# Kernel optimization log

Hardware: AMD Instinct MI355X
Metric: run time of the kernel (lower is better)

The kernel has to match this reference:

```python
import jax, jax.numpy as jnp
import numpy as np

B, S, D, H, DH, FF = 2, 2048, 1024, 16, 64, 4096
EPS = 1e-6


def setup_inputs() -> dict:
    key = jax.random.key(0)
    ks = jax.random.split(key, 12)
    s = lambda fan: 1.0 / np.sqrt(fan)
    return {
        "x": jax.random.normal(ks[0], (B, S, D), dtype=jnp.float32),
        "mask": jax.random.randint(ks[1], (B, S), 0, 2).astype(bool),
        "Wq": jax.random.normal(ks[2], (D, H * DH), dtype=jnp.float32) * s(D),
        "Wk": jax.random.normal(ks[3], (D, H * DH), dtype=jnp.float32) * s(D),
        "Wv": jax.random.normal(ks[4], (D, H * DH), dtype=jnp.float32) * s(D),
        "Wo": jax.random.normal(ks[5], (H * DH, D), dtype=jnp.float32) * s(H * DH),
        "bo": jnp.zeros((D,), dtype=jnp.float32),
        "W1": jax.random.normal(ks[6], (D, FF), dtype=jnp.float32) * s(D),
        "b1": jnp.zeros((FF,), dtype=jnp.float32),
        "W2": jax.random.normal(ks[7], (FF, D), dtype=jnp.float32) * s(FF),
        "b2": jnp.zeros((D,), dtype=jnp.float32),
        "g1": jnp.ones((D,), dtype=jnp.float32),   # layer_norm1 target_std
        "m1": jnp.zeros((D,), dtype=jnp.float32),  # layer_norm1 target_mean
        "g2": jnp.ones((D,), dtype=jnp.float32),
        "m2": jnp.zeros((D,), dtype=jnp.float32),
    }


def layer_norm(x, g, m):
    mu = jnp.mean(x, axis=-1, keepdims=True)
    xc = x - mu
    std = jnp.sqrt(jnp.mean(xc * xc, axis=-1, keepdims=True) + EPS)
    return g * xc / std + m


def reference(x, mask, Wq, Wk, Wv, Wo, bo, W1, b1, W2, b2, g1, m1, g2, m2):
    # --- multi-head self-attention (no proj bias) ---
    q = (x @ Wq).reshape(B, S, H, DH)
    k = (x @ Wk).reshape(B, S, H, DH)
    v = (x @ Wv).reshape(B, S, H, DH)
    scores = jnp.einsum("bqhd,bkhd->bhqk", q, k) / np.sqrt(DH)  # [B,H,S,S]
    scores = jnp.where(mask[:, None, None, :], -jnp.inf, scores)
    att = jax.nn.softmax(scores, axis=-1)
    ctx = jnp.einsum("bhqk,bkhd->bqhd", att, v).reshape(B, S, H * DH)
    attn_out = ctx @ Wo + bo
    # --- post-LN residual block (pre_ln=False, dropouts=0 in eval) ---
    x1 = layer_norm(attn_out + x, g1, m1)
    ff = jax.nn.relu(x1 @ W1 + b1) @ W2 + b2
    return layer_norm(ff + x1, g2, m2)
```

## Files before the change

### kernel.cpp

```cpp
#include <hip/hip_runtime.h>
#include <hip/hip_bf16.h>


typedef __bf16 bf16;
typedef __bf16 bf16x8 __attribute__((ext_vector_type(8)));
typedef __bf16 bf16x4 __attribute__((ext_vector_type(4)));
typedef float  f32x4  __attribute__((ext_vector_type(4)));
typedef float  f32x16 __attribute__((ext_vector_type(16)));
typedef unsigned u32x2 __attribute__((ext_vector_type(2)));
typedef unsigned u32x4 __attribute__((ext_vector_type(4)));

#define DEVI __device__ __forceinline__

constexpr int S_LEN  = 2048;
constexpr int NTOK   = 4096;
constexpr int DMODEL = 1024;
constexpr int NFF    = 4096;
constexpr float SCALE2 = 0.125f * 1.44269504088896f;
constexpr float MASKV2 = -30000.0f;

DEVI void gld16(const void* g, void* l) {
  __builtin_amdgcn_global_load_lds((const __attribute__((address_space(1))) void*)g,
                                   (__attribute__((address_space(3))) void*)l, 16, 0, 0);
}

DEVI f32x4 mfma16(bf16x8 a, bf16x8 b, f32x4 c) {
  return __builtin_amdgcn_mfma_f32_16x16x32_bf16(a, b, c, 0, 0, 0);
}
DEVI f32x16 mfma32(bf16x8 a, bf16x8 b, f32x16 c) {
  return __builtin_amdgcn_mfma_f32_32x32x16_bf16(a, b, c, 0, 0, 0);
}
DEVI unsigned cvtpk(float lo, float hi) {
  unsigned d;
  asm("v_cvt_pk_bf16_f32 %0, %1, %2" : "=v"(d) : "v"(lo), "v"(hi));
  return d;
}
DEVI void plswap(unsigned &a, unsigned &b) {
#if __has_builtin(__builtin_amdgcn_permlane32_swap)
  u32x2 r = __builtin_amdgcn_permlane32_swap(a, b, false, false);
  a = r[0]; b = r[1];
#else
  asm volatile("v_permlane32_swap_b32 %0, %1" : "+v"(a), "+v"(b));
#endif
}
DEVI float fexp2(float x) {
#if __has_builtin(__builtin_amdgcn_exp2f)
  return __builtin_amdgcn_exp2f(x);
#else
  return exp2f(x);
#endif
}
#define M3(a, b, c) fmaxf(fmaxf(a, b), c)

template <int MODE>
__global__ __launch_bounds__(256) void gemm_bt(
    const bf16* __restrict__ A, const bf16* __restrict__ Bt,
    void* __restrict__ out, const float* __restrict__ bias,
    int M, int N, int ld, int Kc, int nx, int ny)
{
  __shared__ bf16 As[128 * 32];
  __shared__ bf16 Bs[128 * 32];
  const int tid  = threadIdx.x;
  const int lane = tid & 63, w = tid >> 6;
  const int wr = w >> 1, wc = w & 1;

  const int id  = blockIdx.x;
  const int xcd = id & 7;
  int t2 = id >> 3;
  const int bx = t2 % nx;  t2 /= nx;
  const int ppx = ny >> 3;
  const int kz = t2 / ppx;
  const int by = xcd * ppx + (t2 % ppx);
  const int brow = by * 128, bcol = bx * 128;

  const bf16* Ag = A  + (size_t)(brow + w * 32 + (lane >> 2)) * ld + kz * Kc + (lane & 3) * 8;
  const bf16* Bg = Bt + (size_t)(bcol + w * 32 + (lane >> 2)) * ld + kz * Kc + (lane & 3) * 8;
  bf16* AsW = As + w * 1024;
  bf16* BsW = Bs + w * 1024;

  f32x4 acc[4][4] = {};

  for (int k0 = 0; k0 < Kc; k0 += 32) {
    gld16(Ag + k0,                    AsW);
    gld16(Ag + k0 + (size_t)16 * ld,  AsW + 512);
    gld16(Bg + k0,                    BsW);
    gld16(Bg + k0 + (size_t)16 * ld,  BsW + 512);
    __syncthreads();

    bf16x8 af[4], bfr[4];
#pragma unroll
    for (int m = 0; m < 4; ++m)
      af[m] = *(const bf16x8*)&As[(wr * 64 + m * 16 + (lane & 15)) * 32 + (lane >> 4) * 8];
#pragma unroll
    for (int n = 0; n < 4; ++n)
      bfr[n] = *(const bf16x8*)&Bs[(wc * 64 + n * 16 + (lane & 15)) * 32 + (lane >> 4) * 8];
    __builtin_amdgcn_s_setprio(1);
#pragma unroll
    for (int m = 0; m < 4; ++m)
#pragma unroll
      for (int n = 0; n < 4; ++n)
        acc[m][n] = mfma16(af[m], bfr[n], acc[m][n]);
    __builtin_amdgcn_s_setprio(0);
    __syncthreads();
  }

  const size_t plane = (size_t)NTOK * DMODEL;
#pragma unroll
  for (int m = 0; m < 4; ++m)
#pragma unroll
    for (int n = 0; n < 4; ++n)
#pragma unroll
      for (int r = 0; r < 4; ++r) {
        const int row = brow + wr * 64 + m * 16 + (lane >> 4) * 4 + r;
        const int col = bcol + wc * 64 + n * 16 + (lane & 15);
        const float v = acc[m][n][r];
        if (MODE == 0) {
          const int b = row >> 11, s = row & 2047;
          const int which = col >> 10, c = col & 1023, h = c >> 6, d = c & 63;
          bf16* qkv = (bf16*)out;
          if (which == 0)
            qkv[(((size_t)(b * 16 + h)) * 2048 + s) * 64 + d] = (bf16)(v * SCALE2);
          else if (which == 1)
            (qkv + plane)[(((size_t)(b * 16 + h)) * 2048 + s) * 64 + d] = (bf16)v;
          else
            (qkv + 2 * plane)[(((size_t)(b * 16 + h)) * 64 + d) * 2048 + s] = (bf16)v;
        } else if (MODE == 3) {
          const float t = v + bias[col];
          ((bf16*)out)[(size_t)row * N + col] = (bf16)fmaxf(t, 0.0f);
        } else {
          ((float*)out)[(size_t)kz * M * N + (size_t)row * N + col] = v;
        }
      }
}

__global__ __launch_bounds__(512) void attn_k(
    const bf16* __restrict__ q, const bf16* __restrict__ k,
    const bf16* __restrict__ vt, const unsigned* __restrict__ mbits,
    bf16* __restrict__ ctx)
{
  __shared__ __align__(16) char smem[36864];
  bf16* Kl = (bf16*)smem;
  bf16* Vl = (bf16*)(smem + 16384);
  const int tid = threadIdx.x, lane = tid & 63, w = tid >> 6;
  const int hi = lane >> 5, li = lane & 31;
  const int id = blockIdx.x;
  const int j = id >> 3;
  const int bh = (id & 7) * 4 + (j & 3);
  const int b = bh >> 4, h = bh & 15;
  const int qbase = (j >> 2) * 256 + w * 32;

  bf16x8 qf[4];
  {
    const bf16* qp = q + ((size_t)bh * S_LEN + qbase + li) * 64 + hi * 8;
#pragma unroll
    for (int c = 0; c < 4; ++c) qf[c] = *(const bf16x8*)(qp + c * 16);
  }
  const u32x4 onesu = {0x3F803F80u, 0x3F803F80u, 0x3F803F80u, 0x3F803F80u};
  const bf16x8 onesv = __builtin_bit_cast(bf16x8, onesu);

  f32x16 o[2] = {};
  f32x16 acc1 = {};
  float mrun = -3.0e38f;

  const int srow = w * 8 + (lane >> 3);
  const int sslot = (lane & 7) ^ ((srow ^ (srow >> 3)) & 7);
  const bf16* kg = k  + ((size_t)bh * S_LEN + srow) * 64 + sslot * 8;
  const bf16* vg = vt + ((size_t)bh * 64 + srow) * S_LEN + sslot * 8;

  gld16(kg, Kl + w * 512);
  gld16(vg, Vl + w * 512);
  __syncthreads();

  int buf = 0;
  for (int kt = 0; kt < 32; ++kt) {
    const int nb = buf ^ 1;
    if (kt + 1 < 32) {
      gld16(kg + (size_t)(kt + 1) * 4096, Kl + nb * 4096 + w * 512);
      gld16(vg + (kt + 1) * 64,           Vl + nb * 4096 + w * 512);
    }
    const unsigned mw0 = mbits[b * 64 + kt * 2]     >> (hi * 4);
    const unsigned mw1 = mbits[b * 64 + kt * 2 + 1] >> (hi * 4);
    const bf16* Kb = Kl + buf * 4096;
    const bf16* Vb = Vl + buf * 4096;

    float sc[2][16];
#pragma unroll
    for (int kblk = 0; kblk < 2; ++kblk) {
      const int key = kblk * 32 + li;
      const unsigned swb = ((key ^ (key >> 3)) & 7) << 4;
      const char* kr = (const char*)Kb + key * 128;
      f32x16 st = {};
      __builtin_amdgcn_s_setprio(1);
#pragma unroll
      for (int c = 0; c < 4; ++c) {
        const bf16x8 kf = *(const bf16x8*)(kr + ((unsigned)(c * 32 + hi * 16) ^ swb));
        st = mfma32(kf, qf[c], st);
      }
      __builtin_amdgcn_s_setprio(0);
      const unsigned msh = kblk ? mw1 : mw0;
#pragma unroll
      for (int r = 0; r < 16; ++r) {
        const int cb = (r & 3) + 8 * (r >> 2);
        sc[kblk][r] = (msh & (1u << cb)) ? MASKV2 : st[r];
      }
    }

    const float* sf = &sc[0][0];
    float m0[11];
#pragma unroll
    for (int i3 = 0; i3 < 10; ++i3) m0[i3] = M3(sf[i3 * 3], sf[i3 * 3 + 1], sf[i3 * 3 + 2]);
    m0[10] = fmaxf(sf[30], sf[31]);
    float tm = fmaxf(fmaxf(M3(m0[0], m0[1], m0[2]), M3(m0[3], m0[4], m0[5])),
                     fmaxf(M3(m0[6], m0[7], m0[8]), fmaxf(m0[9], m0[10])));
    tm = fmaxf(tm, __shfl_xor(tm, 32, 64));

    if (!__all(tm <= mrun + 11.0f)) {
      const float mnew = fmaxf(mrun, tm);
      const float alpha = fexp2(mrun - mnew);
      mrun = mnew;
      o[0] *= alpha;
      o[1] *= alpha;
      acc1[0] = acc1[0] * alpha;
    }
#pragma unroll
    for (int kblk = 0; kblk < 2; ++kblk)
#pragma unroll
      for (int r = 0; r < 16; ++r)
        sc[kblk][r] = fexp2(sc[kblk][r] - mrun);

    bf16x8 pa[4];
#pragma unroll
    for (int kblk = 0; kblk < 2; ++kblk)
#pragma unroll
      for (int hf = 0; hf < 2; ++hf) {
        unsigned A = cvtpk(sc[kblk][hf * 8 + 0], sc[kblk][hf * 8 + 1]);
        unsigned B = cvtpk(sc[kblk][hf * 8 + 2], sc[kblk][hf * 8 + 3]);
        unsigned C = cvtpk(sc[kblk][hf * 8 + 4], sc[kblk][hf * 8 + 5]);
        unsigned D = cvtpk(sc[kblk][hf * 8 + 6], sc[kblk][hf * 8 + 7]);
        plswap(A, C);
        plswap(B, D);
        const u32x4 t = {A, B, C, D};
        pa[kblk * 2 + hf] = __builtin_bit_cast(bf16x8, t);
      }

#pragma unroll
    for (int dblk = 0; dblk < 2; ++dblk) {
      const int d = dblk * 32 + li;
      const unsigned swb = ((d ^ (d >> 3)) & 7) << 4;
      const char* vr = (const char*)Vb + d * 128;
      __builtin_amdgcn_s_setprio(1);
#pragma unroll
      for (int ch = 0; ch < 4; ++ch) {
        const bf16x8 vf = *(const bf16x8*)(vr + ((unsigned)(ch * 32 + hi * 16) ^ swb));
        o[dblk] = mfma32(vf, pa[ch], o[dblk]);
      }
      __builtin_amdgcn_s_setprio(0);
    }
#pragma unroll
    for (int ch = 0; ch < 4; ++ch) acc1 = mfma32(onesv, pa[ch], acc1);
    __syncthreads();
    buf = nb;
  }

  const float rl = 1.0f / acc1[0];
  char* Ep = smem + w * 4608;
#pragma unroll
  for (int dblk = 0; dblk < 2; ++dblk)
#pragma unroll
    for (int g = 0; g < 4; ++g) {
      const unsigned lo = cvtpk(o[dblk][4 * g + 0] * rl, o[dblk][4 * g + 1] * rl);
      const unsigned hw = cvtpk(o[dblk][4 * g + 2] * rl, o[dblk][4 * g + 3] * rl);
      const int d0 = 8 * g + 4 * hi + 32 * dblk;
      *(unsigned long long*)(Ep + li * 144 + d0 * 2) =
          ((unsigned long long)hw << 32) | (unsigned long long)lo;
    }
#pragma unroll
  for (int i = 0; i < 4; ++i) {
    const int r = (lane >> 3) + 8 * i;
    const bf16x8 vv = *(const bf16x8*)(Ep + r * 144 + (lane & 7) * 16);
    *(bf16x8*)(ctx + ((size_t)b * S_LEN + qbase + r) * DMODEL + h * 64 + (lane & 7) * 8) = vv;
  }
}

template <int NPART, int RB>
__global__ __launch_bounds__(256) void ln_k(
    const float* __restrict__ parts, const float* __restrict__ bias,
    const void* __restrict__ resid, const float* __restrict__ gam,
    const float* __restrict__ bet, float* __restrict__ of, bf16* __restrict__ ob)
{
  const int row = blockIdx.x, t = threadIdx.x;
  float4 v = ((const float4*)(parts + (size_t)row * DMODEL))[t];
#pragma unroll
  for (int p = 1; p < NPART; ++p) {
    const float4 u = ((const float4*)(parts + ((size_t)p * NTOK + row) * DMODEL))[t];
    v.x += u.x; v.y += u.y; v.z += u.z; v.w += u.w;
  }
  {
    const float4 b4 = ((const float4*)bias)[t];
    float4 r4;
    if (RB) {
      const bf16x4 rb = *(const bf16x4*)((const bf16*)resid + (size_t)row * DMODEL + t * 4);
      r4.x = (float)rb[0]; r4.y = (float)rb[1]; r4.z = (float)rb[2]; r4.w = (float)rb[3];
    } else {
      r4 = ((const float4*)((const float*)resid + (size_t)row * DMODEL))[t];
    }
    v.x += b4.x + r4.x; v.y += b4.y + r4.y; v.z += b4.z + r4.z; v.w += b4.w + r4.w;
  }
  float s  = v.x + v.y + v.z + v.w;
  float s2 = v.x * v.x + v.y * v.y + v.z * v.z + v.w * v.w;
#pragma unroll
  for (int off = 1; off < 64; off <<= 1) {
    s  += __shfl_xor(s, off, 64);
    s2 += __shfl_xor(s2, off, 64);
  }
  __shared__ float ps[4], ps2[4];
  if ((t & 63) == 0) { ps[t >> 6] = s; ps2[t >> 6] = s2; }
  __syncthreads();
  s  = ps[0] + ps[1] + ps[2] + ps[3];
  s2 = ps2[0] + ps2[1] + ps2[2] + ps2[3];
  const float mu   = s * (1.f / 1024.f);
  const float var  = fmaxf(s2 * (1.f / 1024.f) - mu * mu, 0.f);
  const float rstd = rsqrtf(var + 1e-6f);
  const float4 g4 = ((const float4*)gam)[t];
  const float4 b4 = ((const float4*)bet)[t];
  float4 ov;
  ov.x = g4.x * (v.x - mu) * rstd + b4.x;
  ov.y = g4.y * (v.y - mu) * rstd + b4.y;
  ov.z = g4.z * (v.z - mu) * rstd + b4.z;
  ov.w = g4.w * (v.w - mu) * rstd + b4.w;
  if (of) ((float4*)(of + (size_t)row * DMODEL))[t] = ov;
  if (ob) {
    const bf16x4 o4 = {(bf16)ov.x, (bf16)ov.y, (bf16)ov.z, (bf16)ov.w};
    *(bf16x4*)(ob + (size_t)row * DMODEL + t * 4) = o4;
  }
}

__global__ __launch_bounds__(256) void prep_k(
    const float* __restrict__ x, const float* __restrict__ Wq,
    const float* __restrict__ Wk, const float* __restrict__ Wv,
    const float* __restrict__ Wo, const float* __restrict__ W1,
    const float* __restrict__ W2, const void* __restrict__ mask,
    bf16* __restrict__ xb, bf16* __restrict__ WqkvT, bf16* __restrict__ WoT,
    bf16* __restrict__ W1T, bf16* __restrict__ W2T, unsigned* __restrict__ mbits)
{
  __shared__ float tile[32][33];
  __shared__ int s_gt1, s_f1;
  const int tid = threadIdx.x;
  const int id = blockIdx.x;

  if (id < 4096) {
    const int i = id * 256 + tid;
    const float4 v = ((const float4*)x)[i];
    const bf16x4 o = {(bf16)v.x, (bf16)v.y, (bf16)v.z, (bf16)v.w};
    *(bf16x4*)(xb + (size_t)i * 4) = o;
    return;
  }
  if (id == 16384) {
    if (tid == 0) { s_gt1 = 0; s_f1 = 0; }
    __syncthreads();
    const unsigned* wds = (const unsigned*)mask;
    int gt1 = 0, f1 = 0;
    for (int i = tid; i < 1024; i += 256) {
      const unsigned xw = wds[i];
      gt1 |= (xw > 1u);
      f1  |= (xw == 0x3F800000u);
    }
    if (gt1) atomicOr(&s_gt1, 1);
    if (f1)  atomicOr(&s_f1, 1);
    __syncthreads();
    const int md = s_f1 ? 2 : (s_gt1 ? 1 : 0);
    if (tid < NTOK / 32) {
      unsigned wd = 0;
      for (int jj = 0; jj < 32; ++jj) {
        const int e = tid * 32 + jj;
        unsigned mv;
        if (md == 1)      mv = (((const unsigned char*)mask)[e] != 0);
        else if (md == 2) mv = (((const float*)mask)[e] != 0.f);
        else              mv = (((const int*)mask)[e] != 0);
        wd |= mv << jj;
      }
      mbits[tid] = wd;
    }
    return;
  }
  const float* src; bf16* dst; int K, N, bx, by;
  if (id < 7168) {
    int s2 = id - 4096; const int wq = s2 >> 10; s2 &= 1023;
    src = wq == 0 ? Wq : (wq == 1 ? Wk : Wv);
    dst = WqkvT + (size_t)wq * DMODEL * DMODEL;
    K = 1024; N = 1024; bx = s2 & 31; by = s2 >> 5;
  } else if (id < 8192) {
    const int s2 = id - 7168;
    src = Wo; dst = WoT; K = 1024; N = 1024; bx = s2 & 31; by = s2 >> 5;
  } else if (id < 12288) {
    const int s2 = id - 8192;
    src = W1; dst = W1T; K = 1024; N = 4096; bx = s2 & 127; by = s2 >> 7;
  } else {
    const int s2 = id - 12288;
    src = W2; dst = W2T; K = 4096; N = 1024; bx = s2 & 31; by = s2 >> 5;
  }
  const int tx = tid & 31, ty = tid >> 5;
  const int r0 = by * 32, c0 = bx * 32;
#pragma unroll
  for (int i = 0; i < 32; i += 8)
    tile[ty + i][tx] = src[(size_t)(r0 + ty + i) * N + c0 + tx];
  __syncthreads();
#pragma unroll
  for (int i = 0; i < 32; i += 8)
    dst[(size_t)(c0 + ty + i) * K + r0 + tx] = (bf16)tile[tx][ty + i];
}

extern "C" void kernel_launch(void* const* d_in, const int* in_sizes, int n_in,
                              void* d_out, int out_size, void* d_ws, size_t ws_size,
                              hipStream_t stream)
{
  const float* x    = (const float*)d_in[0];
  const void*  mask = d_in[1];
  const float* Wq   = (const float*)d_in[2];
  const float* Wk   = (const float*)d_in[3];
  const float* Wv   = (const float*)d_in[4];
  const float* Wo   = (const float*)d_in[5];
  const float* bo   = (const float*)d_in[6];
  const float* W1   = (const float*)d_in[7];
  const float* b1   = (const float*)d_in[8];
  const float* W2   = (const float*)d_in[9];
  const float* b2   = (const float*)d_in[10];
  const float* g1   = (const float*)d_in[11];
  const float* m1   = (const float*)d_in[12];
  const float* g2   = (const float*)d_in[13];
  const float* m2   = (const float*)d_in[14];

  const size_t plane = (size_t)NTOK * DMODEL;

  char* ws = (char*)d_ws;
  size_t off = 0;
  auto alloc = [&](size_t bytes) {
    char* p = ws + off;
    off += (bytes + 255) & ~(size_t)255;
    return p;
  };
  bf16* xb     = (bf16*)alloc(plane * 2);
  bf16* WqkvT  = (bf16*)alloc((size_t)3 * DMODEL * DMODEL * 2);
  bf16* WoT    = (bf16*)alloc((size_t)DMODEL * DMODEL * 2);
  bf16* W1T    = (bf16*)alloc((size_t)NFF * DMODEL * 2);
  bf16* W2T    = (bf16*)alloc((size_t)DMODEL * NFF * 2);
  bf16* qkv    = (bf16*)alloc(4 * plane * 2);
  bf16* qb = qkv, *kb = qkv + plane, *vtb = qkv + 2 * plane, *ctxb = qkv + 3 * plane;
  bf16* hb     = qkv;
  float* parts = (float*)alloc(4 * plane * 4);
  bf16*  x1b   = (bf16*)alloc(plane * 2);
  unsigned* maskbits = (unsigned*)alloc(512);

  prep_k<<<dim3(16385), dim3(256), 0, stream>>>(
      x, Wq, Wk, Wv, Wo, W1, W2, mask, xb, WqkvT, WoT, W1T, W2T, maskbits);

  gemm_bt<0><<<dim3(768), dim3(256), 0, stream>>>(
      xb, WqkvT, qkv, nullptr, NTOK, 3 * DMODEL, DMODEL, DMODEL, 24, 32);

  attn_k<<<dim3(256), dim3(512), 0, stream>>>(qb, kb, vtb, maskbits, ctxb);

  gemm_bt<4><<<dim3(1024), dim3(256), 0, stream>>>(
      ctxb, WoT, parts, nullptr, NTOK, DMODEL, DMODEL, DMODEL / 4, 8, 32);
  ln_k<4, 1><<<dim3(NTOK), dim3(256), 0, stream>>>(parts, bo, xb, g1, m1, nullptr, x1b);

  gemm_bt<3><<<dim3(1024), dim3(256), 0, stream>>>(
      x1b, W1T, hb, b1, NTOK, NFF, DMODEL, DMODEL, 32, 32);
  gemm_bt<4><<<dim3(1024), dim3(256), 0, stream>>>(
      hb, W2T, parts, nullptr, NTOK, DMODEL, NFF, NFF / 4, 8, 32);
  ln_k<4, 1><<<dim3(NTOK), dim3(256), 0, stream>>>(parts, b2, x1b, g2, m2, (float*)d_out, nullptr);
}
```

Baseline: 275.5 us.

## Fold attention mask into MFMA bias, halve attention block size, reduce Wo split-K

Precomputes per-key packed bf16 mask biases in prep and injects them into the score accumulator through an extra MFMA with a one-hot operand, replacing the per-element select loop. The attention kernel moves from 512-thread to 256-thread blocks covering 128 queries each, doubling the grid and having each wave load two K/V rows. The Wo projection split-K drops from 4 to 2, with the layernorm reduction adjusted to match. The extra MFMA per key block adds matrix work, and a mask value of -30000 in bf16 relies on the stable softmax path.

```diff
diff --git a/kernel.cpp b/kernel.cpp
--- a/kernel.cpp
+++ b/kernel.cpp
@@ -17,7 +17,6 @@
 constexpr int DMODEL = 1024;
 constexpr int NFF    = 4096;
 constexpr float SCALE2 = 0.125f * 1.44269504088896f;
-constexpr float MASKV2 = -30000.0f;
 
 DEVI void gld16(const void* g, void* l) {
   __builtin_amdgcn_global_load_lds((const __attribute__((address_space(1))) void*)g,
@@ -133,9 +132,9 @@
       }
 }
 
-__global__ __launch_bounds__(512) void attn_k(
+__global__ __launch_bounds__(256) void attn_k(
     const bf16* __restrict__ q, const bf16* __restrict__ k,
-    const bf16* __restrict__ vt, const unsigned* __restrict__ mbits,
+    const bf16* __restrict__ vt, const unsigned* __restrict__ mbp,
     bf16* __restrict__ ctx)
 {
   __shared__ __align__(16) char smem[36864];
@@ -147,7 +146,7 @@
   const int j = id >> 3;
   const int bh = (id & 7) * 4 + (j & 3);
   const int b = bh >> 4, h = bh & 15;
-  const int qbase = (j >> 2) * 256 + w * 32;
+  const int qbase = (j >> 2) * 128 + w * 32;
 
   bf16x8 qf[4];
   {
@@ -157,29 +156,37 @@
   }
   const u32x4 onesu = {0x3F803F80u, 0x3F803F80u, 0x3F803F80u, 0x3F803F80u};
   const bf16x8 onesv = __builtin_bit_cast(bf16x8, onesu);
+  const u32x4 bq1 = {hi ? 0u : 0x3F80u, 0u, 0u, 0u};
+  const bf16x8 bones = __builtin_bit_cast(bf16x8, bq1);
 
   f32x16 o[2] = {};
   f32x16 acc1 = {};
   float mrun = -3.0e38f;
 
-  const int srow = w * 8 + (lane >> 3);
-  const int sslot = (lane & 7) ^ ((srow ^ (srow >> 3)) & 7);
-  const bf16* kg = k  + ((size_t)bh * S_LEN + srow) * 64 + sslot * 8;
-  const bf16* vg = vt + ((size_t)bh * 64 + srow) * S_LEN + sslot * 8;
-
-  gld16(kg, Kl + w * 512);
-  gld16(vg, Vl + w * 512);
+  const int sr0 = w * 16 + (lane >> 3), sr1 = sr0 + 8;
+  const int ss0 = (lane & 7) ^ ((sr0 ^ (sr0 >> 3)) & 7);
+  const int ss1 = (lane & 7) ^ ((sr1 ^ (sr1 >> 3)) & 7);
+  const bf16* kg0 = k  + ((size_t)bh * S_LEN + sr0) * 64 + ss0 * 8;
+  const bf16* kg1 = k  + ((size_t)bh * S_LEN + sr1) * 64 + ss1 * 8;
+  const bf16* vg0 = vt + ((size_t)bh * 64 + sr0) * S_LEN + ss0 * 8;
+  const bf16* vg1 = vt + ((size_t)bh * 64 + sr1) * S_LEN + ss1 * 8;
+
+  gld16(kg0, Kl + w * 1024);
+  gld16(kg1, Kl + w * 1024 + 512);
+  gld16(vg0, Vl + w * 1024);
+  gld16(vg1, Vl + w * 1024 + 512);
   __syncthreads();
 
   int buf = 0;
   for (int kt = 0; kt < 32; ++kt) {
     const int nb = buf ^ 1;
     if (kt + 1 < 32) {
-      gld16(kg + (size_t)(kt + 1) * 4096, Kl + nb * 4096 + w * 512);
-      gld16(vg + (kt + 1) * 64,           Vl + nb * 4096 + w * 512);
-    }
-    const unsigned mw0 = mbits[b * 64 + kt * 2]     >> (hi * 4);
-    const unsigned mw1 = mbits[b * 64 + kt * 2 + 1] >> (hi * 4);
+      gld16(kg0 + (size_t)(kt + 1) * 4096, Kl + nb * 4096 + w * 1024);
+      gld16(kg1 + (size_t)(kt + 1) * 4096, Kl + nb * 4096 + w * 1024 + 512);
+      gld16(vg0 + (kt + 1) * 64,           Vl + nb * 4096 + w * 1024);
+      gld16(vg1 + (kt + 1) * 64,           Vl + nb * 4096 + w * 1024 + 512);
+    }
+    const unsigned mbw = mbp[b * 1024 + kt * 32 + li];
     const bf16* Kb = Kl + buf * 4096;
     const bf16* Vb = Vl + buf * 4096;
 
@@ -189,7 +196,9 @@
       const int key = kblk * 32 + li;
       const unsigned swb = ((key ^ (key >> 3)) & 7) << 4;
       const char* kr = (const char*)Kb + key * 128;
-      f32x16 st = {};
+      const unsigned hw = kblk ? (mbw >> 16) : (mbw & 0xffffu);
+      const u32x4 aq = {hi ? 0u : hw, 0u, 0u, 0u};
+      f32x16 st = mfma32(__builtin_bit_cast(bf16x8, aq), bones, (f32x16){});
       __builtin_amdgcn_s_setprio(1);
 #pragma unroll
       for (int c = 0; c < 4; ++c) {
@@ -197,12 +206,8 @@
         st = mfma32(kf, qf[c], st);
       }
       __builtin_amdgcn_s_setprio(0);
-      const unsigned msh = kblk ? mw1 : mw0;
-#pragma unroll
-      for (int r = 0; r < 16; ++r) {
-        const int cb = (r & 3) + 8 * (r >> 2);
-        sc[kblk][r] = (msh & (1u << cb)) ? MASKV2 : st[r];
-      }
+#pragma unroll
+      for (int r = 0; r < 16; ++r) sc[kblk][r] = st[r];
     }
 
     const float* sf = &sc[0][0];
@@ -341,7 +346,7 @@
     const float* __restrict__ Wo, const float* __restrict__ W1,
     const float* __restrict__ W2, const void* __restrict__ mask,
     bf16* __restrict__ xb, bf16* __restrict__ WqkvT, bf16* __restrict__ WoT,
-    bf16* __restrict__ W1T, bf16* __restrict__ W2T, unsigned* __restrict__ mbits)
+    bf16* __restrict__ W1T, bf16* __restrict__ W2T, unsigned* __restrict__ mbp)
 {
   __shared__ float tile[32][33];
   __shared__ int s_gt1, s_f1;
@@ -369,17 +374,17 @@
     if (f1)  atomicOr(&s_f1, 1);
     __syncthreads();
     const int md = s_f1 ? 2 : (s_gt1 ? 1 : 0);
-    if (tid < NTOK / 32) {
-      unsigned wd = 0;
-      for (int jj = 0; jj < 32; ++jj) {
-        const int e = tid * 32 + jj;
-        unsigned mv;
-        if (md == 1)      mv = (((const unsigned char*)mask)[e] != 0);
-        else if (md == 2) mv = (((const float*)mask)[e] != 0.f);
-        else              mv = (((const int*)mask)[e] != 0);
-        wd |= mv << jj;
-      }
-      mbits[tid] = wd;
+    auto mbit = [&](int e) -> unsigned {
+      if (md == 1)      return (((const unsigned char*)mask)[e] != 0);
+      else if (md == 2) return (((const float*)mask)[e] != 0.f);
+      else              return (((const int*)mask)[e] != 0);
+    };
+    for (int idx = tid; idx < 2048; idx += 256) {
+      const int b = idx >> 10, kt = (idx >> 5) & 31, li = idx & 31;
+      const int base = b * S_LEN + kt * 64 + li;
+      const unsigned h0 = mbit(base)      ? 0xC6EAu : 0u;
+      const unsigned h1 = mbit(base + 32) ? 0xC6EAu : 0u;
+      mbp[idx] = h0 | (h1 << 16);
     }
     return;
   }
@@ -449,19 +454,19 @@
   bf16* hb     = qkv;
   float* parts = (float*)alloc(4 * plane * 4);
   bf16*  x1b   = (bf16*)alloc(plane * 2);
-  unsigned* maskbits = (unsigned*)alloc(512);
+  unsigned* mbp = (unsigned*)alloc(8192);
 
   prep_k<<<dim3(16385), dim3(256), 0, stream>>>(
-      x, Wq, Wk, Wv, Wo, W1, W2, mask, xb, WqkvT, WoT, W1T, W2T, maskbits);
+      x, Wq, Wk, Wv, Wo, W1, W2, mask, xb, WqkvT, WoT, W1T, W2T, mbp);
 
   gemm_bt<0><<<dim3(768), dim3(256), 0, stream>>>(
       xb, WqkvT, qkv, nullptr, NTOK, 3 * DMODEL, DMODEL, DMODEL, 24, 32);
 
-  attn_k<<<dim3(256), dim3(512), 0, stream>>>(qb, kb, vtb, maskbits, ctxb);
-
-  gemm_bt<4><<<dim3(1024), dim3(256), 0, stream>>>(
-      ctxb, WoT, parts, nullptr, NTOK, DMODEL, DMODEL, DMODEL / 4, 8, 32);
-  ln_k<4, 1><<<dim3(NTOK), dim3(256), 0, stream>>>(parts, bo, xb, g1, m1, nullptr, x1b);
+  attn_k<<<dim3(512), dim3(256), 0, stream>>>(qb, kb, vtb, mbp, ctxb);
+
+  gemm_bt<4><<<dim3(512), dim3(256), 0, stream>>>(
+      ctxb, WoT, parts, nullptr, NTOK, DMODEL, DMODEL, DMODEL / 2, 8, 32);
+  ln_k<2, 1><<<dim3(NTOK), dim3(256), 0, stream>>>(parts, bo, xb, g1, m1, nullptr, x1b);
 
   gemm_bt<3><<<dim3(1024), dim3(256), 0, stream>>>(
       x1b, W1T, hb, b1, NTOK, NFF, DMODEL, DMODEL, 32, 32);
```

New measurement: 268.3 us. -2.6%, faster.
